# Optimization experiments

Hardware: AMD Instinct MI355X
Metric: run time of the kernel (lower is better)

## Reference

```python
import jax, jax.numpy as jnp
import numpy as np

B, N, D = 4, 16384, 128       # batch, tokens (mesh points), input_dim
H, DH = 8, 64                 # heads, dim_head
INNER = H * DH


def setup_inputs() -> dict:
    key = jax.random.key(0)
    ks = jax.random.split(key, 7)
    s = 0.02  # weight init scale
    return {
        "queries": jax.random.normal(ks[0], (B, N, D), jnp.float32),
        "keys":    jax.random.normal(ks[1], (B, N, D), jnp.float32),
        "values":  jax.random.normal(ks[2], (B, N, D), jnp.float32),
        "Wq": jax.random.normal(ks[3], (INNER, D), jnp.float32) * s,
        "Wk": jax.random.normal(ks[4], (INNER, D), jnp.float32) * s,
        "Wo": jax.random.normal(ks[5], (D, INNER), jnp.float32) * s,
        "bo": jnp.zeros((D,), jnp.float32),
    }


def _split_heads(x, b, n):
    # [b, n, h*d] -> [b, h, n, d]
    return x.reshape(b, n, H, DH).transpose(0, 2, 1, 3)


def reference(queries, keys, values, Wq, Wk, Wo, bo):
    b, n, _ = queries.shape
    q = _split_heads(queries @ Wq.T, b, n)
    k = _split_heads(keys    @ Wk.T, b, n)
    # NOTE: original source applies to_k to values (bug kept for faithfulness)
    v = _split_heads(values  @ Wk.T, b, n)
    # Galerkin linear attention, associative order: q @ (k^T v) / n.
    # (In the runnable no-mask path the instance norms are computed but
    #  discarded by the original code, so they are omitted here.)
    dots = jnp.einsum('bhnd,bhne->bhde', k, v)          # [b,h,d,d]
    out = jnp.einsum('bhnd,bhde->bhne', q, dots) / n    # [b,h,n,d]
    out = out.transpose(0, 2, 1, 3).reshape(b, n, INNER)
    return out @ Wo.T + bo
```

## Files before the change

kernel.cpp:

```cpp
#include <hip/hip_runtime.h>
#include <hip/hip_bf16.h>

#define BB    4
#define NN    16384
#define DD    128
#define HH    8
#define DHH   64
#define INNER 512
#define PC    128

typedef __attribute__((ext_vector_type(8))) short bf16x8;
typedef __attribute__((ext_vector_type(4))) short short4_t;
typedef __attribute__((ext_vector_type(4))) float f32x4;
typedef unsigned short ushort_t;

#define MFMA(a, b, c) __builtin_amdgcn_mfma_f32_16x16x32_bf16((a), (b), (c), 0, 0, 0)

__device__ __forceinline__ short f2bf(float x) {
    union { float f; unsigned u; } v; v.f = x;
    unsigned u = v.u;
    u += 0x7fffu + ((u >> 16) & 1u);
    return (short)(u >> 16);
}

__device__ __forceinline__ float bf2f(ushort_t us) {
    union { unsigned u; float f; } v;
    v.u = ((unsigned)us) << 16;
    return v.f;
}

__device__ __forceinline__ bf16x8 load_row8(const float* __restrict__ p) {
    f32x4 a = *(const f32x4*)p;
    f32x4 b = *(const f32x4*)(p + 4);
    bf16x8 r;
    r[0] = f2bf(a[0]); r[1] = f2bf(a[1]); r[2] = f2bf(a[2]); r[3] = f2bf(a[3]);
    r[4] = f2bf(b[0]); r[5] = f2bf(b[1]); r[6] = f2bf(b[2]); r[7] = f2bf(b[3]);
    return r;
}

__device__ __forceinline__ bf16x8 load_col8(const float* __restrict__ p, int stride) {
    bf16x8 r;
#pragma unroll
    for (int j = 0; j < 8; ++j) r[j] = f2bf(p[(size_t)j * stride]);
    return r;
}

__global__ __launch_bounds__(512, 4) void k1_partialS_ab(
        const float* __restrict__ keys, const float* __restrict__ vals,
        const float* __restrict__ Wq, const float* __restrict__ Wk,
        const float* __restrict__ Wo,
        ushort_t* __restrict__ partial, ushort_t* __restrict__ Abf,
        ushort_t* __restrict__ BTbf) {
    const int lane = threadIdx.x & 63;
    const int w    = threadIdx.x >> 6;
    const int ml   = lane & 15;
    const int quad = lane >> 4;

    __shared__ short tK[2][32][132];
    __shared__ short tV[2][32][132];

    if (blockIdx.x < BB * PC) {
        const int b     = blockIdx.x >> 7;
        const int chunk = blockIdx.x & (PC - 1);
        const int r0    = chunk * (NN / PC);
        const int mw    = w & 3;
        const int nw    = w >> 2;

        const float* kbase = keys + (size_t)b * NN * DD;
        const float* vbase = vals + (size_t)b * NN * DD;

        const int lin0 = (int)threadIdx.x;
        const int ca0  = (2 * mw + 0) * 16 + ml;
        const int ca1  = (2 * mw + 1) * 16 + ml;

        f32x4 acc[2][4];
#pragma unroll
        for (int i = 0; i < 2; ++i)
#pragma unroll
            for (int t = 0; t < 4; ++t) acc[i][t] = (f32x4){0.f, 0.f, 0.f, 0.f};

        {
            const float* kp = kbase + (size_t)r0 * DD;
            const float* vp = vbase + (size_t)r0 * DD;
#pragma unroll
            for (int it = 0; it < 2; ++it) {
                const int lin = lin0 + it * 512;
                const int row = lin >> 5;
                const int c4  = (lin & 31) << 2;
                f32x4 kk = *(const f32x4*)(kp + (size_t)row * DD + c4);
                f32x4 vv = *(const f32x4*)(vp + (size_t)row * DD + c4);
                short4_t ks, vs;
#pragma unroll
                for (int j = 0; j < 4; ++j) { ks[j] = f2bf(kk[j]); vs[j] = f2bf(vv[j]); }
                *(short4_t*)&tK[0][row][c4] = ks;
                *(short4_t*)&tV[0][row][c4] = vs;
            }
        }
        __syncthreads();

        for (int s = 0; s < 4; ++s) {
            const int cur   = s & 1;
            const bool more = (s < 3);

            f32x4 kreg[2], vreg[2];
            if (more) {
                const float* kp = kbase + (size_t)(r0 + (s + 1) * 32) * DD;
                const float* vp = vbase + (size_t)(r0 + (s + 1) * 32) * DD;
#pragma unroll
                for (int it = 0; it < 2; ++it) {
                    const int lin = lin0 + it * 512;
                    const int row = lin >> 5;
                    const int c4  = (lin & 31) << 2;
                    kreg[it] = *(const f32x4*)(kp + (size_t)row * DD + c4);
                    vreg[it] = *(const f32x4*)(vp + (size_t)row * DD + c4);
                }
            }

            {
                bf16x8 a0, a1;
#pragma unroll
                for (int j = 0; j < 8; ++j) {
                    a0[j] = tK[cur][quad * 8 + j][ca0];
                    a1[j] = tK[cur][quad * 8 + j][ca1];
                }
#pragma unroll
                for (int t = 0; t < 4; ++t) {
                    const int cb = (nw * 4 + t) * 16 + ml;
                    bf16x8 bf;
#pragma unroll
                    for (int j = 0; j < 8; ++j) bf[j] = tV[cur][quad * 8 + j][cb];
                    acc[0][t] = MFMA(a0, bf, acc[0][t]);
                    acc[1][t] = MFMA(a1, bf, acc[1][t]);
                }
            }

            if (more) {
                __syncthreads();
                const int nb = cur ^ 1;
#pragma unroll
                for (int it = 0; it < 2; ++it) {
                    const int lin = lin0 + it * 512;
                    const int row = lin >> 5;
                    const int c4  = (lin & 31) << 2;
                    short4_t ks, vs;
#pragma unroll
                    for (int j = 0; j < 4; ++j) {
                        ks[j] = f2bf(kreg[it][j]);
                        vs[j] = f2bf(vreg[it][j]);
                    }
                    *(short4_t*)&tK[nb][row][c4] = ks;
                    *(short4_t*)&tV[nb][row][c4] = vs;
                }
                __syncthreads();
            }
        }

        ushort_t* outp = partial + (size_t)blockIdx.x * DD * DD;
#pragma unroll
        for (int i = 0; i < 2; ++i) {
            const int mrow = (2 * mw + i) * 16 + quad * 4;
#pragma unroll
            for (int t = 0; t < 4; ++t) {
                const int col = (nw * 4 + t) * 16 + ml;
#pragma unroll
                for (int r = 0; r < 4; ++r)
                    outp[(size_t)(mrow + r) * DD + col] = (ushort_t)f2bf(acc[i][t][r]);
            }
        }
    } else {
        const int ab    = blockIdx.x - BB * PC;
        const int h     = ab & 7;
        const int which = ab >> 3;
        const float* Wkh = Wk + (size_t)h * DHH * DD;

        f32x4 acc[8];
#pragma unroll
        for (int t = 0; t < 8; ++t) acc[t] = (f32x4){0.f, 0.f, 0.f, 0.f};

        if (which == 0) {
            const float* Wqh = Wq + (size_t)h * DHH * DD;
#pragma unroll
            for (int kc = 0; kc < 2; ++kc) {
                const int d0 = kc * 32 + quad * 8;
                bf16x8 a = load_col8(Wqh + (size_t)d0 * DD + w * 16 + ml, DD);
#pragma unroll
                for (int t = 0; t < 8; ++t) {
                    bf16x8 bf = load_col8(Wkh + (size_t)d0 * DD + t * 16 + ml, DD);
                    acc[t] = MFMA(a, bf, acc[t]);
                }
            }
            ushort_t* dst = Abf + (size_t)h * DD * DD;
#pragma unroll
            for (int t = 0; t < 8; ++t)
#pragma unroll
                for (int r = 0; r < 4; ++r)
                    dst[(size_t)(w * 16 + quad * 4 + r) * DD + t * 16 + ml] =
                        (ushort_t)f2bf(acc[t][r]);
        } else {
#pragma unroll
            for (int kc = 0; kc < 2; ++kc) {
                const int e0 = kc * 32 + quad * 8;
                bf16x8 a = load_row8(Wo + (size_t)(w * 16 + ml) * INNER + h * DHH + e0);
#pragma unroll
                for (int t = 0; t < 8; ++t) {
                    bf16x8 bf = load_col8(Wkh + (size_t)e0 * DD + t * 16 + ml, DD);
                    acc[t] = MFMA(a, bf, acc[t]);
                }
            }
            ushort_t* dst = BTbf + (size_t)h * DD * DD;
#pragma unroll
            for (int t = 0; t < 8; ++t)
#pragma unroll
                for (int r = 0; r < 4; ++r)
                    dst[(size_t)(w * 16 + quad * 4 + r) * DD + t * 16 + ml] =
                        (ushort_t)f2bf(acc[t][r]);
        }
    }
}

__global__ __launch_bounds__(256) void k2_reduce(
        const ushort_t* __restrict__ partial, float* __restrict__ S,
        float* __restrict__ G) {
    const int tid = blockIdx.x * 256 + threadIdx.x;
    const int e   = tid * 2;
    const int b   = e >> 14;
    const int idx = e & 16383;
    const unsigned* p32 =
        (const unsigned*)(partial + ((size_t)b * PC) * DD * DD + idx);
    float s0 = 0.f, s1 = 0.f;
#pragma unroll 16
    for (int c = 0; c < PC; ++c) {
        const unsigned u = p32[(size_t)c * (DD * DD / 2)];
        s0 += bf2f((ushort_t)(u & 0xffffu));
        s1 += bf2f((ushort_t)(u >> 16));
    }
    S[e] = s0;  S[e + 1] = s1;
    G[e] = 0.f; G[e + 1] = 0.f;
}

__global__ __launch_bounds__(512) void k3_middle(
        const float* __restrict__ S, const ushort_t* __restrict__ Abf,
        const ushort_t* __restrict__ BTbf, float* __restrict__ G) {
    const int b    = blockIdx.x >> 3;
    const int h    = blockIdx.x & 7;
    const int lane = threadIdx.x & 63;
    const int w    = threadIdx.x >> 6;
    const int ml   = lane & 15;
    const int quad = lane >> 4;

    __shared__ short ST[128 * 136];
    __shared__ short T [128 * 136];

    const float*    Sb = S    + (size_t)b * DD * DD;
    const ushort_t* Ah = Abf  + (size_t)h * DD * DD;
    const ushort_t* Bh = BTbf + (size_t)h * DD * DD;

#pragma unroll
    for (int it = 0; it < 8; ++it) {
        const int idx4 = ((int)threadIdx.x + it * 512) * 4;
        const int c  = idx4 >> 7;
        const int cp = idx4 & 127;
        f32x4 v = *(const f32x4*)(Sb + idx4);
#pragma unroll
        for (int j = 0; j < 4; ++j) ST[(cp + j) * 136 + c] = f2bf(v[j]);
    }
    __syncthreads();

    {
        f32x4 acc[8];
#pragma unroll
        for (int t = 0; t < 8; ++t) acc[t] = (f32x4){0.f, 0.f, 0.f, 0.f};
#pragma unroll
        for (int kc = 0; kc < 4; ++kc) {
            const int c0 = kc * 32 + quad * 8;
            bf16x8 a = *(const bf16x8*)&Ah[(size_t)(w * 16 + ml) * DD + c0];
#pragma unroll
            for (int t = 0; t < 8; ++t) {
                bf16x8 bf = *(const bf16x8*)&ST[(t * 16 + ml) * 136 + c0];
                acc[t] = MFMA(a, bf, acc[t]);
            }
        }
#pragma unroll
        for (int t = 0; t < 8; ++t)
#pragma unroll
            for (int r = 0; r < 4; ++r)
                T[(w * 16 + quad * 4 + r) * 136 + t * 16 + ml] = f2bf(acc[t][r]);
    }
    __syncthreads();

    {
        f32x4 acc[8];
#pragma unroll
        for (int t = 0; t < 8; ++t) acc[t] = (f32x4){0.f, 0.f, 0.f, 0.f};
#pragma unroll
        for (int kc = 0; kc < 4; ++kc) {
            const int k0 = kc * 32 + quad * 8;
            bf16x8 a = *(const bf16x8*)&T[(w * 16 + ml) * 136 + k0];
#pragma unroll
            for (int t = 0; t < 8; ++t) {
                bf16x8 bf = *(const bf16x8*)&Bh[(size_t)(t * 16 + ml) * DD + k0];
                acc[t] = MFMA(a, bf, acc[t]);
            }
        }
        float* Gb = G + (size_t)b * DD * DD;
#pragma unroll
        for (int t = 0; t < 8; ++t)
#pragma unroll
            for (int r = 0; r < 4; ++r)
                atomicAdd(&Gb[(w * 16 + quad * 4 + r) * DD + t * 16 + ml],
                          acc[t][r]);
    }
}

__global__ __launch_bounds__(512, 4) void k4_final(
        const float* __restrict__ queries, const float* __restrict__ G,
        const float* __restrict__ bo, float* __restrict__ outp) {
    const int b  = blockIdx.x >> 7;
    const int r0 = (blockIdx.x & 127) * 128;

    __shared__ short Gt[128 * 136];
    {
        const float* Gb = G + (size_t)b * DD * DD;
        const float invN = 6.103515625e-05f;
#pragma unroll 4
        for (int it = 0; it < 32; ++it) {
            const int idx = (int)threadIdx.x + it * 512;
            const int cp = idx >> 7, c = idx & 127;
            Gt[c * 136 + cp] = f2bf(Gb[idx] * invN);
        }
    }
    __syncthreads();

    const int lane = threadIdx.x & 63;
    const int w    = threadIdx.x >> 6;
    const int ml   = lane & 15;
    const int quad = lane >> 4;
    const float* qbase = queries + ((size_t)b * NN + r0) * DD;

    f32x4 acc[8];
#pragma unroll
    for (int t = 0; t < 8; ++t) acc[t] = (f32x4){0.f, 0.f, 0.f, 0.f};

#pragma unroll
    for (int kc = 0; kc < 4; ++kc) {
        const int k0 = kc * 32 + quad * 8;
        bf16x8 a = load_row8(qbase + (size_t)(w * 16 + ml) * DD + k0);
#pragma unroll
        for (int t = 0; t < 8; ++t) {
            bf16x8 bf = *(const bf16x8*)&Gt[(t * 16 + ml) * 136 + k0];
            acc[t] = MFMA(a, bf, acc[t]);
        }
    }

    float* ob = outp + ((size_t)b * NN + r0) * DD;
#pragma unroll
    for (int t = 0; t < 8; ++t) {
        const int c = t * 16 + ml;
        const float boc = bo[c];
#pragma unroll
        for (int r = 0; r < 4; ++r)
            ob[(size_t)(w * 16 + quad * 4 + r) * DD + c] = acc[t][r] + boc;
    }
}

extern "C" void kernel_launch(void* const* d_in, const int* in_sizes, int n_in,
                              void* d_out, int out_size, void* d_ws, size_t ws_size,
                              hipStream_t stream) {
    const float* queries = (const float*)d_in[0];
    const float* keys    = (const float*)d_in[1];
    const float* values  = (const float*)d_in[2];
    const float* Wq      = (const float*)d_in[3];
    const float* Wk      = (const float*)d_in[4];
    const float* Wo      = (const float*)d_in[5];
    const float* bo      = (const float*)d_in[6];
    float* out = (float*)d_out;

    float* S = (float*)d_ws;
    float* G = S + (size_t)BB * DD * DD;
    ushort_t* Abf     = (ushort_t*)(G + (size_t)BB * DD * DD);
    ushort_t* BTbf    = Abf  + (size_t)HH * DD * DD;
    ushort_t* partial = BTbf + (size_t)HH * DD * DD;

    hipLaunchKernelGGL(k1_partialS_ab, dim3(BB * PC + 16), dim3(512), 0, stream,
                       keys, values, Wq, Wk, Wo, partial, Abf, BTbf);
    hipLaunchKernelGGL(k2_reduce, dim3(128), dim3(256), 0, stream,
                       partial, S, G);
    hipLaunchKernelGGL(k3_middle, dim3(BB * HH), dim3(512), 0, stream,
                       S, Abf, BTbf, G);
    hipLaunchKernelGGL(k4_final, dim3(512), dim3(512), 0, stream,
                       queries, G, bo, out);
}
```

Before: 169.9 us.

## Split middle kernel into row tiles and emit transposed bf16 S from reduce

The reduce kernel now writes S directly as a transposed bf16 matrix, so the middle kernel no longer loads fp32 S and transposes it in shared memory. The middle kernel's grid grows from 32 to 128 blocks: each block computes a 32-row slice of A·S^T·B^T, with each warp owning a 16x32 output tile. This is meant to raise occupancy on a kernel that previously used only 32 workgroups, and to cut shared-memory traffic. In exchange, the reduce kernel's transposed stores are uncoalesced, and each block reads S from global memory rather than shared memory.

```diff
diff --git a/kernel.cpp b/kernel.cpp
--- a/kernel.cpp
+++ b/kernel.cpp
@@ -219,7 +219,7 @@
 }
 
 __global__ __launch_bounds__(256) void k2_reduce(
-        const ushort_t* __restrict__ partial, float* __restrict__ S,
+        const ushort_t* __restrict__ partial, ushort_t* __restrict__ SbfT,
         float* __restrict__ G) {
     const int tid = blockIdx.x * 256 + threadIdx.x;
     const int e   = tid * 2;
@@ -234,80 +234,80 @@
         s0 += bf2f((ushort_t)(u & 0xffffu));
         s1 += bf2f((ushort_t)(u >> 16));
     }
-    S[e] = s0;  S[e + 1] = s1;
+    const int c  = idx >> 7;
+    const int cp = idx & 127;
+    ushort_t* st = SbfT + (size_t)b * DD * DD;
+    st[(size_t)(cp    ) * DD + c] = (ushort_t)f2bf(s0);
+    st[(size_t)(cp + 1) * DD + c] = (ushort_t)f2bf(s1);
     G[e] = 0.f; G[e + 1] = 0.f;
 }
 
 __global__ __launch_bounds__(512) void k3_middle(
-        const float* __restrict__ S, const ushort_t* __restrict__ Abf,
+        const ushort_t* __restrict__ SbfT, const ushort_t* __restrict__ Abf,
         const ushort_t* __restrict__ BTbf, float* __restrict__ G) {
-    const int b    = blockIdx.x >> 3;
-    const int h    = blockIdx.x & 7;
+    const int bi = blockIdx.x;
+    const int b  = bi >> 5;
+    const int h  = (bi >> 2) & 7;
+    const int m0 = (bi & 3) * 32;
     const int lane = threadIdx.x & 63;
     const int w    = threadIdx.x >> 6;
     const int ml   = lane & 15;
     const int quad = lane >> 4;
-
-    __shared__ short ST[128 * 136];
-    __shared__ short T [128 * 136];
-
-    const float*    Sb = S    + (size_t)b * DD * DD;
+    const int mt   = w & 1;
+    const int nh   = w >> 1;
+
+    __shared__ short T[32 * 136];
+
+    const ushort_t* Sb = SbfT + (size_t)b * DD * DD;
     const ushort_t* Ah = Abf  + (size_t)h * DD * DD;
     const ushort_t* Bh = BTbf + (size_t)h * DD * DD;
 
-#pragma unroll
-    for (int it = 0; it < 8; ++it) {
-        const int idx4 = ((int)threadIdx.x + it * 512) * 4;
-        const int c  = idx4 >> 7;
-        const int cp = idx4 & 127;
-        f32x4 v = *(const f32x4*)(Sb + idx4);
-#pragma unroll
-        for (int j = 0; j < 4; ++j) ST[(cp + j) * 136 + c] = f2bf(v[j]);
-    }
-    __syncthreads();
-
     {
-        f32x4 acc[8];
-#pragma unroll
-        for (int t = 0; t < 8; ++t) acc[t] = (f32x4){0.f, 0.f, 0.f, 0.f};
+        f32x4 acc[2];
+        acc[0] = (f32x4){0.f, 0.f, 0.f, 0.f};
+        acc[1] = (f32x4){0.f, 0.f, 0.f, 0.f};
 #pragma unroll
         for (int kc = 0; kc < 4; ++kc) {
             const int c0 = kc * 32 + quad * 8;
-            bf16x8 a = *(const bf16x8*)&Ah[(size_t)(w * 16 + ml) * DD + c0];
-#pragma unroll
-            for (int t = 0; t < 8; ++t) {
-                bf16x8 bf = *(const bf16x8*)&ST[(t * 16 + ml) * 136 + c0];
+            bf16x8 a = *(const bf16x8*)&Ah[(size_t)(m0 + mt * 16 + ml) * DD + c0];
+#pragma unroll
+            for (int t = 0; t < 2; ++t) {
+                const int n = (2 * nh + t) * 16 + ml;
+                bf16x8 bf = *(const bf16x8*)&Sb[(size_t)n * DD + c0];
                 acc[t] = MFMA(a, bf, acc[t]);
             }
         }
 #pragma unroll
-        for (int t = 0; t < 8; ++t)
+        for (int t = 0; t < 2; ++t)
 #pragma unroll
             for (int r = 0; r < 4; ++r)
-                T[(w * 16 + quad * 4 + r) * 136 + t * 16 + ml] = f2bf(acc[t][r]);
+                T[(mt * 16 + quad * 4 + r) * 136 + (2 * nh + t) * 16 + ml] =
+                    f2bf(acc[t][r]);
     }
     __syncthreads();
 
     {
-        f32x4 acc[8];
-#pragma unroll
-        for (int t = 0; t < 8; ++t) acc[t] = (f32x4){0.f, 0.f, 0.f, 0.f};
+        f32x4 acc[2];
+        acc[0] = (f32x4){0.f, 0.f, 0.f, 0.f};
+        acc[1] = (f32x4){0.f, 0.f, 0.f, 0.f};
 #pragma unroll
         for (int kc = 0; kc < 4; ++kc) {
             const int k0 = kc * 32 + quad * 8;
-            bf16x8 a = *(const bf16x8*)&T[(w * 16 + ml) * 136 + k0];
-#pragma unroll
-            for (int t = 0; t < 8; ++t) {
-                bf16x8 bf = *(const bf16x8*)&Bh[(size_t)(t * 16 + ml) * DD + k0];
+            bf16x8 a = *(const bf16x8*)&T[(mt * 16 + ml) * 136 + k0];
+#pragma unroll
+            for (int t = 0; t < 2; ++t) {
+                const int n = (2 * nh + t) * 16 + ml;
+                bf16x8 bf = *(const bf16x8*)&Bh[(size_t)n * DD + k0];
                 acc[t] = MFMA(a, bf, acc[t]);
             }
         }
         float* Gb = G + (size_t)b * DD * DD;
 #pragma unroll
-        for (int t = 0; t < 8; ++t)
+        for (int t = 0; t < 2; ++t)
 #pragma unroll
             for (int r = 0; r < 4; ++r)
-                atomicAdd(&Gb[(w * 16 + quad * 4 + r) * DD + t * 16 + ml],
+                atomicAdd(&Gb[(m0 + mt * 16 + quad * 4 + r) * DD +
+                              (2 * nh + t) * 16 + ml],
                           acc[t][r]);
     }
 }
@@ -375,8 +375,8 @@
     const float* bo      = (const float*)d_in[6];
     float* out = (float*)d_out;
 
-    float* S = (float*)d_ws;
-    float* G = S + (size_t)BB * DD * DD;
+    ushort_t* SbfT = (ushort_t*)d_ws;
+    float* G = (float*)d_ws + (size_t)BB * DD * DD;
     ushort_t* Abf     = (ushort_t*)(G + (size_t)BB * DD * DD);
     ushort_t* BTbf    = Abf  + (size_t)HH * DD * DD;
     ushort_t* partial = BTbf + (size_t)HH * DD * DD;
@@ -384,9 +384,9 @@
     hipLaunchKernelGGL(k1_partialS_ab, dim3(BB * PC + 16), dim3(512), 0, stream,
                        keys, values, Wq, Wk, Wo, partial, Abf, BTbf);
     hipLaunchKernelGGL(k2_reduce, dim3(128), dim3(256), 0, stream,
-                       partial, S, G);
-    hipLaunchKernelGGL(k3_middle, dim3(BB * HH), dim3(512), 0, stream,
-                       S, Abf, BTbf, G);
+                       partial, SbfT, G);
+    hipLaunchKernelGGL(k3_middle, dim3(128), dim3(512), 0, stream,
+                       SbfT, Abf, BTbf, G);
     hipLaunchKernelGGL(k4_final, dim3(512), dim3(512), 0, stream,
                        queries, G, bo, out);
 }
```

New measurement: 163.0 us. -4.1%, faster.
